# Performance work log

Measured on AMD Instinct MI355X. Metric: run time of the kernel, lower is better.

The kernel has to match this reference:

```python
import jax, jax.numpy as jnp
import numpy as np

B, H, T, D = 4, 16, 4096, 64
N_TASKS, K_LEN = 8, 128


def setup_inputs() -> dict:
    key = jax.random.key(0)
    ks = jax.random.split(key, 6)
    x = jax.random.normal(ks[0], (B, H, T, D), dtype=jnp.float32)
    q = jax.random.normal(ks[1], (B, H, T, D), dtype=jnp.float32)
    kv_k = jax.random.normal(ks[2], (N_TASKS, H, K_LEN, D), dtype=jnp.float32)
    kv_v = jax.random.normal(ks[3], (N_TASKS, H, K_LEN, D), dtype=jnp.float32)
    gates = jax.random.uniform(ks[4], (N_TASKS,), dtype=jnp.float32)
    trk_id = jax.random.randint(ks[5], (B, T), 0, N_TASKS, dtype=jnp.int64)
    return {"x": x, "q": q, "kv_k": kv_k, "kv_v": kv_v, "gates": gates, "trk_id": trk_id}


def reference(x, q, kv_k, kv_v, gates, trk_id):
    # Faithful to ICLAdaptor.fn: per-task SDPA of each token's query against
    # that task's (k, v) adaptor memory, scaled by a learned gate, scattered
    # back by trk_id, residual-added to x. Ragged torch gather/scatter is
    # expressed as masked per-task dense attention (small fixed n_tasks loop).
    d = q.shape[-1]
    scale = jnp.asarray(1.0, q.dtype) / jnp.sqrt(jnp.asarray(d, q.dtype))
    n_tasks = kv_k.shape[0]
    dx = jnp.zeros_like(q)
    for i in range(n_tasks):
        # scores: [b, h, t, k_len]
        s = jnp.einsum('bhtd,hkd->bhtk', q, kv_k[i]) * scale
        a = jax.nn.softmax(s, axis=-1)
        o = jnp.einsum('bhtk,hkd->bhtd', a, kv_v[i]) * gates[i]
        mask = (trk_id == i)[:, None, :, None]  # [b,1,t,1]
        dx = dx + jnp.where(mask, o, jnp.zeros((), o.dtype))
    return x + dx
```

## Files before the change

kernel.cpp:

```cpp
#include <hip/hip_runtime.h>

#define B_   4
#define H_   16
#define T_   4096
#define D_   64
#define KL_  128
#define NT_  8
#define NTOK (B_ * T_)
#define CAP  4096

typedef __bf16 bf16;
typedef __attribute__((ext_vector_type(8))) __bf16 bf16x8;
typedef __attribute__((ext_vector_type(4))) __bf16 bf16x4;
typedef __attribute__((ext_vector_type(4))) float  floatx4;


__global__ void zero_counts_k(int* __restrict__ ws) {
    if (threadIdx.x < NT_) ws[threadIdx.x] = 0;
}

__global__ void scatter_tokens_k(const int* __restrict__ trk, int* __restrict__ ws) {
    int* counts = ws;
    int* bucket = ws + NT_;
    int idx  = blockIdx.x * blockDim.x + threadIdx.x;
    int lane = threadIdx.x & 63;
    int task = (idx < NTOK) ? trk[idx] : -1;
    unsigned long long mymask = 0ull;
    int myCnt = 0;
#pragma unroll
    for (int i = 0; i < NT_; i++) {
        unsigned long long m = __ballot(task == i);
        if (task == i) mymask = m;
        if (lane == i) myCnt = (int)__popcll(m);
    }
    int b0 = 0;
    if (lane < NT_) b0 = atomicAdd(&counts[lane], myCnt);
    int myBase = __shfl(b0, (task < 0) ? 0 : task);
    if (idx < NTOK) {
        int pos = myBase + (int)__popcll(mymask & ((1ull << lane) - 1ull));
        bucket[task * CAP + pos] = idx;
    }
}

__global__ __launch_bounds__(256) void attn_k(
    const float* __restrict__ q,   const float* __restrict__ kvk,
    const float* __restrict__ kvv, const float* __restrict__ gates,
    const float* __restrict__ x,   float* __restrict__ out,
    const int* __restrict__ ws)
{
    __shared__ bf16 Kl[KL_ * 72];
    __shared__ bf16 Vt[D_ * 136];
    __shared__ bf16 Pl[4][16 * 136];

    const int task = blockIdx.z, h = blockIdx.y, chunk = blockIdx.x;
    const int cnt = ws[task];
    if (cnt == 0) return;
    const int* bucket = ws + NT_ + task * CAP;
    const float gate = gates[task];

    {
        const size_t kvbase = (size_t)(task * H_ + h) * (KL_ * D_ / 4);
        const float4* kf = (const float4*)kvk + kvbase;
        const float4* vf = (const float4*)kvv + kvbase;
        for (int ii = threadIdx.x; ii < KL_ * D_ / 4; ii += 256) {
            int k = ii >> 4, d4 = ii & 15;
            float4 a = kf[ii];
            bf16x4 w; w[0]=(bf16)a.x; w[1]=(bf16)a.y; w[2]=(bf16)a.z; w[3]=(bf16)a.w;
            *(bf16x4*)&Kl[k * 72 + d4 * 4] = w;
            float4 v = vf[ii];
            int d = d4 * 4;
            Vt[(d+0)*136 + k] = (bf16)v.x;
            Vt[(d+1)*136 + k] = (bf16)v.y;
            Vt[(d+2)*136 + k] = (bf16)v.z;
            Vt[(d+3)*136 + k] = (bf16)v.w;
        }
    }
    __syncthreads();

    const int wave = threadIdx.x >> 6;
    const int lane = threadIdx.x & 63;
    const int c = lane & 15, quad = lane >> 4;
    bf16* Pw = &Pl[wave][0];

    for (int ts = chunk * 4 + wave; ts * 16 < cnt; ts += 32) {
        int slotc = ts * 16 + c;
        int tokc  = bucket[slotc < cnt ? slotc : cnt - 1];
        int bb = tokc >> 12, tt = tokc & (T_ - 1);
        const float4* qf = (const float4*)q + ((size_t)((bb * H_ + h) * T_ + tt) * (D_ / 4));
        bf16x8 aq[2];
#pragma unroll
        for (int dc = 0; dc < 2; dc++) {
            float4 f0 = qf[dc * 8 + quad * 2];
            float4 f1 = qf[dc * 8 + quad * 2 + 1];
            aq[dc][0]=(bf16)f0.x; aq[dc][1]=(bf16)f0.y; aq[dc][2]=(bf16)f0.z; aq[dc][3]=(bf16)f0.w;
            aq[dc][4]=(bf16)f1.x; aq[dc][5]=(bf16)f1.y; aq[dc][6]=(bf16)f1.z; aq[dc][7]=(bf16)f1.w;
        }
        floatx4 sc[8];
#pragma unroll
        for (int nt = 0; nt < 8; nt++) {
            floatx4 z = {0.f, 0.f, 0.f, 0.f};
            sc[nt] = z;
#pragma unroll
            for (int dc = 0; dc < 2; dc++) {
                bf16x8 bk = *(const bf16x8*)&Kl[(nt * 16 + c) * 72 + dc * 32 + quad * 8];
                sc[nt] = __builtin_amdgcn_mfma_f32_16x16x32_bf16(aq[dc], bk, sc[nt], 0, 0, 0);
            }
        }
        float mx[4], lsum[4];
#pragma unroll
        for (int r = 0; r < 4; r++) {
            float m = -1e30f;
#pragma unroll
            for (int nt = 0; nt < 8; nt++) m = fmaxf(m, sc[nt][r]);
#pragma unroll
            for (int off = 1; off < 16; off <<= 1) m = fmaxf(m, __shfl_xor(m, off));
            mx[r] = m;
        }
#pragma unroll
        for (int r = 0; r < 4; r++) {
            float sum = 0.f;
#pragma unroll
            for (int nt = 0; nt < 8; nt++) {
                float p = exp2f((sc[nt][r] - mx[r]) * 0.18033688011112042f);
                sc[nt][r] = p;
                sum += p;
            }
#pragma unroll
            for (int off = 1; off < 16; off <<= 1) sum += __shfl_xor(sum, off);
            lsum[r] = sum;
        }
#pragma unroll
        for (int nt = 0; nt < 8; nt++)
#pragma unroll
            for (int r = 0; r < 4; r++)
                Pw[(quad * 4 + r) * 136 + nt * 16 + c] = (bf16)sc[nt][r];
        floatx4 acc[4];
#pragma unroll
        for (int dt = 0; dt < 4; dt++) { floatx4 z = {0.f,0.f,0.f,0.f}; acc[dt] = z; }
#pragma unroll
        for (int kc = 0; kc < 4; kc++) {
            bf16x8 ap = *(const bf16x8*)&Pw[c * 136 + kc * 32 + quad * 8];
#pragma unroll
            for (int dt = 0; dt < 4; dt++) {
                bf16x8 bv = *(const bf16x8*)&Vt[(dt * 16 + c) * 136 + kc * 32 + quad * 8];
                acc[dt] = __builtin_amdgcn_mfma_f32_16x16x32_bf16(ap, bv, acc[dt], 0, 0, 0);
            }
        }
#pragma unroll
        for (int r = 0; r < 4; r++) {
            int slot = ts * 16 + quad * 4 + r;
            if (slot < cnt) {
                int tok = bucket[slot];
                int b2 = tok >> 12, t2 = tok & (T_ - 1);
                float scale = gate / lsum[r];
                int base = ((b2 * H_ + h) * T_ + t2) * D_;
#pragma unroll
                for (int dt = 0; dt < 4; dt++) {
                    int off = base + dt * 16 + c;
                    out[off] = x[off] + acc[dt][r] * scale;
                }
            }
        }
    }
}

extern "C" void kernel_launch(void* const* d_in, const int* in_sizes, int n_in,
                              void* d_out, int out_size, void* d_ws, size_t ws_size,
                              hipStream_t stream) {
    const float* x     = (const float*)d_in[0];
    const float* q     = (const float*)d_in[1];
    const float* kvk   = (const float*)d_in[2];
    const float* kvv   = (const float*)d_in[3];
    const float* gates = (const float*)d_in[4];
    const int*   trk   = (const int*)d_in[5];
    float* out = (float*)d_out;
    int* ws = (int*)d_ws;

    zero_counts_k<<<1, 64, 0, stream>>>(ws);
    scatter_tokens_k<<<NTOK / 256, 256, 0, stream>>>(trk, ws);
    attn_k<<<dim3(8, H_, NT_), 256, 0, stream>>>(q, kvk, kvv, gates, x, out, ws);
}
```

Measured before the change: 240.5 us.

## Transpose MFMA operands to keep softmax probabilities in registers via shuffles

Swaps the MFMA operand order so each lane holds one token's scores across keys. Softmax then reduces with two cross-quad shuffles, and the probabilities are packed into bf16 registers and redistributed with __shfl instead of a round-trip through LDS. The output becomes contiguous float4 stores per token, with x prefetched earlier. The change also removes the P shared buffer, adds a launch_bounds occupancy hint and replaces the zeroing kernel with hipMemsetAsync. In exchange it adds many shuffles and selects per kc step, which raises register pressure.

```diff
diff --git a/kernel.cpp b/kernel.cpp
--- a/kernel.cpp
+++ b/kernel.cpp
@@ -14,10 +14,6 @@
 typedef __attribute__((ext_vector_type(4))) __bf16 bf16x4;
 typedef __attribute__((ext_vector_type(4))) float  floatx4;
 
-
-__global__ void zero_counts_k(int* __restrict__ ws) {
-    if (threadIdx.x < NT_) ws[threadIdx.x] = 0;
-}
 
 __global__ void scatter_tokens_k(const int* __restrict__ trk, int* __restrict__ ws) {
     int* counts = ws;
@@ -42,7 +38,7 @@
     }
 }
 
-__global__ __launch_bounds__(256) void attn_k(
+__global__ __launch_bounds__(256, 4) void attn_k(
     const float* __restrict__ q,   const float* __restrict__ kvk,
     const float* __restrict__ kvv, const float* __restrict__ gates,
     const float* __restrict__ x,   float* __restrict__ out,
@@ -50,7 +46,6 @@
 {
     __shared__ bf16 Kl[KL_ * 72];
     __shared__ bf16 Vt[D_ * 136];
-    __shared__ bf16 Pl[4][16 * 136];
 
     const int task = blockIdx.z, h = blockIdx.y, chunk = blockIdx.x;
     const int cnt = ws[task];
@@ -80,20 +75,20 @@
     const int wave = threadIdx.x >> 6;
     const int lane = threadIdx.x & 63;
     const int c = lane & 15, quad = lane >> 4;
-    bf16* Pw = &Pl[wave][0];
 
     for (int ts = chunk * 4 + wave; ts * 16 < cnt; ts += 32) {
-        int slotc = ts * 16 + c;
-        int tokc  = bucket[slotc < cnt ? slotc : cnt - 1];
-        int bb = tokc >> 12, tt = tokc & (T_ - 1);
-        const float4* qf = (const float4*)q + ((size_t)((bb * H_ + h) * T_ + tt) * (D_ / 4));
-        bf16x8 aq[2];
+        int slot = ts * 16 + c;
+        int tok  = bucket[slot < cnt ? slot : cnt - 1];
+        int bb = tok >> 12, tt = tok & (T_ - 1);
+        const size_t tbase = (size_t)((bb * H_ + h) * T_ + tt) * (D_ / 4);
+        const float4* qf = (const float4*)q + tbase;
+        bf16x8 bq[2];
 #pragma unroll
         for (int dc = 0; dc < 2; dc++) {
             float4 f0 = qf[dc * 8 + quad * 2];
             float4 f1 = qf[dc * 8 + quad * 2 + 1];
-            aq[dc][0]=(bf16)f0.x; aq[dc][1]=(bf16)f0.y; aq[dc][2]=(bf16)f0.z; aq[dc][3]=(bf16)f0.w;
-            aq[dc][4]=(bf16)f1.x; aq[dc][5]=(bf16)f1.y; aq[dc][6]=(bf16)f1.z; aq[dc][7]=(bf16)f1.w;
+            bq[dc][0]=(bf16)f0.x; bq[dc][1]=(bf16)f0.y; bq[dc][2]=(bf16)f0.z; bq[dc][3]=(bf16)f0.w;
+            bq[dc][4]=(bf16)f1.x; bq[dc][5]=(bf16)f1.y; bq[dc][6]=(bf16)f1.z; bq[dc][7]=(bf16)f1.w;
         }
         floatx4 sc[8];
 #pragma unroll
@@ -102,63 +97,72 @@
             sc[nt] = z;
 #pragma unroll
             for (int dc = 0; dc < 2; dc++) {
-                bf16x8 bk = *(const bf16x8*)&Kl[(nt * 16 + c) * 72 + dc * 32 + quad * 8];
-                sc[nt] = __builtin_amdgcn_mfma_f32_16x16x32_bf16(aq[dc], bk, sc[nt], 0, 0, 0);
+                bf16x8 ak = *(const bf16x8*)&Kl[(nt * 16 + c) * 72 + dc * 32 + quad * 8];
+                sc[nt] = __builtin_amdgcn_mfma_f32_16x16x32_bf16(ak, bq[dc], sc[nt], 0, 0, 0);
             }
         }
-        float mx[4], lsum[4];
-#pragma unroll
-        for (int r = 0; r < 4; r++) {
-            float m = -1e30f;
-#pragma unroll
-            for (int nt = 0; nt < 8; nt++) m = fmaxf(m, sc[nt][r]);
-#pragma unroll
-            for (int off = 1; off < 16; off <<= 1) m = fmaxf(m, __shfl_xor(m, off));
-            mx[r] = m;
-        }
-#pragma unroll
-        for (int r = 0; r < 4; r++) {
-            float sum = 0.f;
-#pragma unroll
-            for (int nt = 0; nt < 8; nt++) {
-                float p = exp2f((sc[nt][r] - mx[r]) * 0.18033688011112042f);
-                sc[nt][r] = p;
-                sum += p;
-            }
-#pragma unroll
-            for (int off = 1; off < 16; off <<= 1) sum += __shfl_xor(sum, off);
-            lsum[r] = sum;
-        }
+        float m = -1e30f;
 #pragma unroll
         for (int nt = 0; nt < 8; nt++)
 #pragma unroll
-            for (int r = 0; r < 4; r++)
-                Pw[(quad * 4 + r) * 136 + nt * 16 + c] = (bf16)sc[nt][r];
+            for (int r = 0; r < 4; r++) m = fmaxf(m, sc[nt][r]);
+        m = fmaxf(m, __shfl_xor(m, 16));
+        m = fmaxf(m, __shfl_xor(m, 32));
+        float sum = 0.f;
+        int pblo[8], pbhi[8];
+#pragma unroll
+        for (int nt = 0; nt < 8; nt++) {
+            union { bf16x4 v; int2 i; } u;
+#pragma unroll
+            for (int r = 0; r < 4; r++) {
+                float p = exp2f((sc[nt][r] - m) * 0.18033688011112042f);
+                sum += p;
+                u.v[r] = (bf16)p;
+            }
+            pblo[nt] = u.i.x; pbhi[nt] = u.i.y;
+        }
+        sum += __shfl_xor(sum, 16);
+        sum += __shfl_xor(sum, 32);
+
+        const float4* xb = (const float4*)x + tbase;
+        float4 xv[4];
+#pragma unroll
+        for (int dt = 0; dt < 4; dt++) xv[dt] = xb[dt * 4 + quad];
+
         floatx4 acc[4];
 #pragma unroll
         for (int dt = 0; dt < 4; dt++) { floatx4 z = {0.f,0.f,0.f,0.f}; acc[dt] = z; }
+        const int srcA = ((quad & 1) << 5) + c;
+        const int srcB = srcA + 16;
+        const bool useB = (quad >= 2);
 #pragma unroll
         for (int kc = 0; kc < 4; kc++) {
-            bf16x8 ap = *(const bf16x8*)&Pw[c * 136 + kc * 32 + quad * 8];
+            int a0 = __shfl(pblo[2*kc],   srcA), b0 = __shfl(pblo[2*kc+1], srcA);
+            int a1 = __shfl(pbhi[2*kc],   srcA), b1 = __shfl(pbhi[2*kc+1], srcA);
+            int a2 = __shfl(pblo[2*kc],   srcB), b2 = __shfl(pblo[2*kc+1], srcB);
+            int a3 = __shfl(pbhi[2*kc],   srcB), b3 = __shfl(pbhi[2*kc+1], srcB);
+            union { bf16x8 v; int4 i; } pf;
+            pf.i.x = useB ? b0 : a0;
+            pf.i.y = useB ? b1 : a1;
+            pf.i.z = useB ? b2 : a2;
+            pf.i.w = useB ? b3 : a3;
 #pragma unroll
             for (int dt = 0; dt < 4; dt++) {
-                bf16x8 bv = *(const bf16x8*)&Vt[(dt * 16 + c) * 136 + kc * 32 + quad * 8];
-                acc[dt] = __builtin_amdgcn_mfma_f32_16x16x32_bf16(ap, bv, acc[dt], 0, 0, 0);
+                bf16x8 av = *(const bf16x8*)&Vt[(dt * 16 + c) * 136 + kc * 32 + quad * 8];
+                acc[dt] = __builtin_amdgcn_mfma_f32_16x16x32_bf16(av, pf.v, acc[dt], 0, 0, 0);
             }
         }
+        if (slot < cnt) {
+            float scale = gate / sum;
+            float4* ob = (float4*)out + tbase;
 #pragma unroll
-        for (int r = 0; r < 4; r++) {
-            int slot = ts * 16 + quad * 4 + r;
-            if (slot < cnt) {
-                int tok = bucket[slot];
-                int b2 = tok >> 12, t2 = tok & (T_ - 1);
-                float scale = gate / lsum[r];
-                int base = ((b2 * H_ + h) * T_ + t2) * D_;
-#pragma unroll
-                for (int dt = 0; dt < 4; dt++) {
-                    int off = base + dt * 16 + c;
-                    out[off] = x[off] + acc[dt][r] * scale;
-                }
+            for (int dt = 0; dt < 4; dt++) {
+                float4 o;
+                o.x = xv[dt].x + acc[dt][0] * scale;
+                o.y = xv[dt].y + acc[dt][1] * scale;
+                o.z = xv[dt].z + acc[dt][2] * scale;
+                o.w = xv[dt].w + acc[dt][3] * scale;
+                ob[dt * 4 + quad] = o;
             }
         }
     }
@@ -176,7 +180,7 @@
     float* out = (float*)d_out;
     int* ws = (int*)d_ws;
 
-    zero_counts_k<<<1, 64, 0, stream>>>(ws);
+    hipMemsetAsync(ws, 0, NT_ * sizeof(int), stream);
     scatter_tokens_k<<<NTOK / 256, 256, 0, stream>>>(trk, ws);
     attn_k<<<dim3(8, H_, NT_), 256, 0, stream>>>(q, kvk, kvv, gates, x, out, ws);
 }
```

Measured after the change: 253.5 us. +5.4%, slower.
